# Kernel tuning notes

Hardware: AMD Instinct MI355X
Metric: run time of the kernel (lower is better)

Reference implementation:

```python
import jax, jax.numpy as jnp
import numpy as np

N_NODES = 75000
N_EDGES = 1200000
DIM = 64


def setup_inputs() -> dict:
    key = jax.random.key(0)
    ks = jax.random.split(key, 9)
    d_u = jax.random.normal(ks[0], (N_NODES, DIM), dtype=jnp.float32)
    p_u = jax.random.normal(ks[1], (N_NODES, DIM), dtype=jnp.float32)
    s = 1.0 / np.sqrt(DIM)
    w_q = jax.random.normal(ks[2], (DIM, DIM), dtype=jnp.float32) * s
    w_k = jax.random.normal(ks[3], (DIM, DIM), dtype=jnp.float32) * s
    w_v = jax.random.normal(ks[4], (DIM, DIM), dtype=jnp.float32) * s
    e1 = jax.random.normal(ks[5], (DIM,), dtype=jnp.float32) * s
    e2 = jax.random.normal(ks[6], (DIM,), dtype=jnp.float32) * s
    src = jax.random.randint(ks[7], (N_EDGES,), 0, N_NODES, dtype=jnp.int32)
    dst = jax.random.randint(ks[8], (N_EDGES,), 0, N_NODES, dtype=jnp.int32)
    return {"d_u": d_u, "p_u": p_u, "w_q": w_q, "w_k": w_k, "w_v": w_v,
            "e1": e1, "e2": e2, "src": src, "dst": dst}


def reference(d_u, p_u, w_q, w_k, w_v, e1, e2, src, dst):
    n_nodes = d_u.shape[0]
    # per-node edge scores: e1(w_k(p_u)) on src side, e2(w_q(d_u)) on dst side
    h_src = (p_u @ w_k.T) @ e1            # [N]
    h_dst = (d_u @ w_q.T) @ e2            # [N]
    # apply_edges(u_add_v): c_e = h_src[u] + h_dst[v], shape [E]
    c = h_src[src] + h_dst[dst]
    # EdgeWeightNorm(norm='right'): divide by sum of incoming edge weights at dst
    denom = jax.ops.segment_sum(c, dst, num_segments=n_nodes)  # [N]
    c = c / denom[dst]
    # update_all(u_mul_e, sum): messages w_v(p_u)[u] * c_e, summed at dst
    wv = p_u @ w_v.T                      # [N, D]
    msg = wv[src] * c[:, None]            # [E, D]
    out = jax.ops.segment_sum(msg, dst, num_segments=n_nodes)  # [N, D]
    return out
```

## Files before the change

### kernel.cpp

```cpp
#include <hip/hip_runtime.h>

#define N_NODES 75000
#define N_EDGES 1200000
#define DIM 64
#define SCAN_BLK 1024
#define N_SCAN_BLKS ((N_NODES + SCAN_BLK - 1) / SCAN_BLK)
#define NCOPY 8
#define HIST_BLKS ((N_EDGES + 1023) / 1024)
#define NW_BLKS 1024
#define FAT_BLKS (HIST_BLKS + NW_BLKS)

__device__ __forceinline__ float lane_bcf(float v, int l) {
    return __int_as_float(__builtin_amdgcn_readlane(__float_as_int(v), l));
}
__device__ __forceinline__ int lane_bci(int v, int l) {
    return __builtin_amdgcn_readlane(v, l);
}

__global__ __launch_bounds__(256, 4) void fat_kernel(
    const int* __restrict__ dst, int* __restrict__ cnt8, int* __restrict__ rank,
    const float* __restrict__ d_u, const float* __restrict__ p_u,
    const float* __restrict__ w_v, const float* __restrict__ w_q,
    const float* __restrict__ w_k,
    const float* __restrict__ e1, const float* __restrict__ e2,
    double* __restrict__ h_src, double* __restrict__ h_dst,
    float* __restrict__ wv_out) {

    if (blockIdx.x < HIST_BLKS) {
        int base = blockIdx.x << 10;
        int* mycnt = cnt8 + (size_t)(blockIdx.x & (NCOPY - 1)) * N_NODES;
        #pragma unroll
        for (int k = 0; k < 4; ++k) {
            int e = base + k * 256 + threadIdx.x;
            if (e < N_EDGES) {
                int d = __builtin_nontemporal_load(&dst[e]);
                int r = atomicAdd(&mycnt[d], 1);
                __builtin_nontemporal_store(r, &rank[e]);
            }
        }
        return;
    }

    __shared__ double al_sh[DIM];
    __shared__ double bl_sh[DIM];
    int lane = threadIdx.x & 63;

    if (threadIdx.x < DIM) {
        double al = 0.0, bl = 0.0;
        #pragma unroll 8
        for (int j = 0; j < DIM; ++j) {
            al += (double)e1[j] * (double)w_k[j * DIM + threadIdx.x];
            bl += (double)e2[j] * (double)w_q[j * DIM + threadIdx.x];
        }
        al_sh[threadIdx.x] = al;
        bl_sh[threadIdx.x] = bl;
    }

    float w[DIM];
    const float4* wr = (const float4*)(w_v + (size_t)lane * DIM);
    #pragma unroll
    for (int k = 0; k < DIM / 4; ++k) {
        float4 v = wr[k];
        w[4 * k + 0] = v.x; w[4 * k + 1] = v.y;
        w[4 * k + 2] = v.z; w[4 * k + 3] = v.w;
    }
    __syncthreads();
    double al = al_sh[lane];
    double bl = bl_sh[lane];

    int wave = ((blockIdx.x - HIST_BLKS) * 256 + threadIdx.x) >> 6;
    int nwaves = NW_BLKS * 4;

    for (int i = wave; i < N_NODES; i += nwaves) {
        float pl = __builtin_nontemporal_load(&p_u[(size_t)i * DIM + lane]);
        float dl = __builtin_nontemporal_load(&d_u[(size_t)i * DIM + lane]);

        double hs = (double)pl * al;
        #pragma unroll
        for (int off = 32; off > 0; off >>= 1) hs += __shfl_xor(hs, off, 64);
        double hd = (double)dl * bl;
        #pragma unroll
        for (int off = 32; off > 0; off >>= 1) hd += __shfl_xor(hd, off, 64);
        if (lane == 0) {
            __builtin_nontemporal_store(hs, &h_src[i]);
            __builtin_nontemporal_store(hd, &h_dst[i]);
        }

        float a0 = 0.f, a1 = 0.f, a2 = 0.f, a3 = 0.f;
        #pragma unroll
        for (int d = 0; d < DIM; d += 4) {
            a0 += w[d + 0] * lane_bcf(pl, d + 0);
            a1 += w[d + 1] * lane_bcf(pl, d + 1);
            a2 += w[d + 2] * lane_bcf(pl, d + 2);
            a3 += w[d + 3] * lane_bcf(pl, d + 3);
        }
        __builtin_nontemporal_store((a0 + a1) + (a2 + a3),
                                    &wv_out[(size_t)i * DIM + lane]);
    }
}

__global__ __launch_bounds__(SCAN_BLK) void scan1_kernel(
    int* __restrict__ cnt8, int* __restrict__ cnt,
    int* __restrict__ row, int* __restrict__ bsum) {
    __shared__ int sh[SCAN_BLK];
    int tid = threadIdx.x;
    int i = blockIdx.x * SCAN_BLK + tid;
    int v = 0;
    if (i < N_NODES) {
        int run = 0;
        #pragma unroll
        for (int c = 0; c < NCOPY; ++c) {
            int x = cnt8[(size_t)c * N_NODES + i];
            cnt8[(size_t)c * N_NODES + i] = run;
            run += x;
        }
        v = run;
        cnt[i] = run;
    }
    sh[tid] = v;
    __syncthreads();
    for (int off = 1; off < SCAN_BLK; off <<= 1) {
        int t = (tid >= off) ? sh[tid - off] : 0;
        __syncthreads();
        sh[tid] += t;
        __syncthreads();
    }
    if (i < N_NODES) row[i] = sh[tid] - v;
    if (tid == SCAN_BLK - 1) bsum[blockIdx.x] = sh[tid];
}

__global__ __launch_bounds__(256) void scan23_kernel(
    int* __restrict__ row, const int* __restrict__ bsum) {
    __shared__ int pref[N_SCAN_BLKS];
    int tid = threadIdx.x;
    if (tid == 0) {
        int run = 0;
        #pragma unroll 8
        for (int k = 0; k < N_SCAN_BLKS; ++k) { pref[k] = run; run += bsum[k]; }
    }
    __syncthreads();
    int i = blockIdx.x * 256 + tid;
    if (i >= N_NODES) return;
    row[i] += pref[i / SCAN_BLK];
}

__global__ __launch_bounds__(256) void build_kernel(
    const int* __restrict__ src, const int* __restrict__ dst,
    const int* __restrict__ row, const int* __restrict__ cnt8,
    const int* __restrict__ rank, int* __restrict__ csr_src) {
    int e = blockIdx.x * 256 + threadIdx.x;
    if (e >= N_EDGES) return;
    int d = dst[e];
    int copy = (e >> 10) & (NCOPY - 1);
    int pos = row[d] + cnt8[(size_t)copy * N_NODES + d] + rank[e];
    csr_src[pos] = src[e];
}

__global__ __launch_bounds__(256) void node_gather(
    const int* __restrict__ row, const int* __restrict__ cnt,
    const int* __restrict__ csr_src,
    const double* __restrict__ h_src, const double* __restrict__ h_dst,
    const float* __restrict__ wv, float* __restrict__ out) {
    int gtid = blockIdx.x * 256 + threadIdx.x;
    int node = gtid >> 6;
    int lane = threadIdx.x & 63;
    if (node >= N_NODES) return;

    int start = row[node];
    int deg = cnt[node];
    double hd = h_dst[node];

    if (deg <= 64) {
        int s0 = 0;
        double c0 = 0.0;
        if (lane < deg) {
            s0 = csr_src[start + lane];
            c0 = h_src[s0] + hd;
        }
        double r = c0;
        if (deg > 32) r += __shfl_xor(r, 32, 64);
        if (deg > 16) r += __shfl_xor(r, 16, 64);
        r += __shfl_xor(r, 8, 64);
        r += __shfl_xor(r, 4, 64);
        r += __shfl_xor(r, 2, 64);
        r += __shfl_xor(r, 1, 64);
        double inv = 1.0 / r;
        float cf0 = (lane < deg) ? (float)(c0 * inv) : 0.f;

        int g = lane >> 4;
        int sub = lane & 15;
        float ax = 0.f, ay = 0.f, az = 0.f, aw = 0.f;
        int rounds = (deg + 3) >> 2;
        int j = 0;
        for (; j + 2 <= rounds; j += 2) {
            int l0 = 4 * j + g;
            int l1 = l0 + 4;
            int   sA = __shfl(s0, l0, 64);
            float cA = __shfl(cf0, l0, 64);
            int   sB = __shfl(s0, l1, 64);
            float cB = __shfl(cf0, l1, 64);
            float4 vA = ((const float4*)(wv + (size_t)sA * DIM))[sub];
            float4 vB = ((const float4*)(wv + (size_t)sB * DIM))[sub];
            ax += vA.x * cA; ay += vA.y * cA; az += vA.z * cA; aw += vA.w * cA;
            ax += vB.x * cB; ay += vB.y * cB; az += vB.z * cB; aw += vB.w * cB;
        }
        if (j < rounds) {
            int l0 = 4 * j + g;
            int   sA = __shfl(s0, l0, 64);
            float cA = __shfl(cf0, l0, 64);
            float4 vA = ((const float4*)(wv + (size_t)sA * DIM))[sub];
            ax += vA.x * cA; ay += vA.y * cA; az += vA.z * cA; aw += vA.w * cA;
        }
        ax += __shfl_xor(ax, 16, 64); ay += __shfl_xor(ay, 16, 64);
        az += __shfl_xor(az, 16, 64); aw += __shfl_xor(aw, 16, 64);
        ax += __shfl_xor(ax, 32, 64); ay += __shfl_xor(ay, 32, 64);
        az += __shfl_xor(az, 32, 64); aw += __shfl_xor(aw, 32, 64);
        if (g == 0) {
            float4 o; o.x = ax; o.y = ay; o.z = az; o.w = aw;
            ((float4*)(out + (size_t)node * DIM))[sub] = o;
        }
    } else {
        double denom = 0.0;
        for (int base = 0; base < deg; base += 64) {
            int m = deg - base; if (m > 64) m = 64;
            double c = 0.0;
            if (lane < m) {
                int s = csr_src[start + base + lane];
                c = h_src[s] + hd;
            }
            #pragma unroll
            for (int off = 32; off > 0; off >>= 1) c += __shfl_xor(c, off, 64);
            denom += c;
        }
        double inv = 1.0 / denom;
        float acc = 0.f;
        for (int base = 0; base < deg; base += 64) {
            int m = deg - base; if (m > 64) m = 64;
            int s1 = 0; float cf1 = 0.f;
            if (lane < m) {
                s1 = csr_src[start + base + lane];
                cf1 = (float)((h_src[s1] + hd) * inv);
            }
            for (int j = 0; j < m; ++j) {
                int s = lane_bci(s1, j);
                float cf = lane_bcf(cf1, j);
                acc += wv[(size_t)s * DIM + lane] * cf;
            }
        }
        out[(size_t)node * DIM + lane] = acc;
    }
}

extern "C" void kernel_launch(void* const* d_in, const int* in_sizes, int n_in,
                              void* d_out, int out_size, void* d_ws, size_t ws_size,
                              hipStream_t stream) {
    const float* d_u = (const float*)d_in[0];
    const float* p_u = (const float*)d_in[1];
    const float* w_q = (const float*)d_in[2];
    const float* w_k = (const float*)d_in[3];
    const float* w_v = (const float*)d_in[4];
    const float* e1  = (const float*)d_in[5];
    const float* e2  = (const float*)d_in[6];
    const int*   src = (const int*)d_in[7];
    const int*   dst = (const int*)d_in[8];
    float* out = (float*)d_out;

    double* h_src  = (double*)d_ws;
    double* h_dst  = h_src + N_NODES;
    float*  wv     = (float*)(h_dst + N_NODES);
    int*    cnt    = (int*)(wv + (size_t)N_NODES * DIM);
    int*    row    = cnt + N_NODES;
    int*    bsum   = row + N_NODES;
    int*    cnt8   = bsum + 128;
    int*    rank   = cnt8 + (size_t)NCOPY * N_NODES;
    int*    csr_src= rank + N_EDGES;

    hipMemsetAsync(cnt8, 0, sizeof(int) * (size_t)NCOPY * N_NODES, stream);

    fat_kernel<<<FAT_BLKS, 256, 0, stream>>>(
        dst, cnt8, rank, d_u, p_u, w_v, w_q, w_k, e1, e2, h_src, h_dst, wv);

    scan1_kernel<<<N_SCAN_BLKS, SCAN_BLK, 0, stream>>>(cnt8, cnt, row, bsum);
    scan23_kernel<<<(N_NODES + 255) / 256, 256, 0, stream>>>(row, bsum);

    build_kernel<<<(N_EDGES + 255) / 256, 256, 0, stream>>>(
        src, dst, row, cnt8, rank, csr_src);

    node_gather<<<(N_NODES * 64 + 255) / 256, 256, 0, stream>>>(
        row, cnt, csr_src, h_src, h_dst, wv, out);
}
```

Before: 274.2 us.

## Use XCC-local histogram copies, interleave block roles, fuse scan passes

Histogram blocks now select their counter copy by the hardware XCC ID, so atomics from one chiplet stay on that chiplet's copy, and the copy index is packed into the rank's top bits for the build step. Histogram and node-work blocks are interleaved 2:1 so both kinds of work are spread across the device. The two scan kernels are merged into one single-pass scan where each block publishes its sum with a flag and later blocks spin on earlier ones. Nontemporal hints are removed in several places. The spin wait assumes earlier blocks are scheduled first, which risks a deadlock if they are not.

```diff
diff --git a/kernel.cpp b/kernel.cpp
--- a/kernel.cpp
+++ b/kernel.cpp
@@ -6,8 +6,8 @@
 #define SCAN_BLK 1024
 #define N_SCAN_BLKS ((N_NODES + SCAN_BLK - 1) / SCAN_BLK)
 #define NCOPY 8
-#define HIST_BLKS ((N_EDGES + 1023) / 1024)
-#define NW_BLKS 1024
+#define HIST_BLKS 1172
+#define NW_BLKS 586
 #define FAT_BLKS (HIST_BLKS + NW_BLKS)
 
 __device__ __forceinline__ float lane_bcf(float v, int l) {
@@ -26,16 +26,24 @@
     double* __restrict__ h_src, double* __restrict__ h_dst,
     float* __restrict__ wv_out) {
 
-    if (blockIdx.x < HIST_BLKS) {
-        int base = blockIdx.x << 10;
-        int* mycnt = cnt8 + (size_t)(blockIdx.x & (NCOPY - 1)) * N_NODES;
+    int b = blockIdx.x;
+    int g = b / 3;
+    int r = b - 3 * g;
+
+    if (r < 2) {
+        int hb = 2 * g + r;
+        int xcc;
+        asm volatile("s_getreg_b32 %0, hwreg(HW_REG_XCC_ID)" : "=s"(xcc));
+        xcc &= (NCOPY - 1);
+        int* mycnt = cnt8 + (size_t)xcc * N_NODES;
+        int tag = xcc << 28;
+        int base = hb << 10;
         #pragma unroll
         for (int k = 0; k < 4; ++k) {
             int e = base + k * 256 + threadIdx.x;
             if (e < N_EDGES) {
-                int d = __builtin_nontemporal_load(&dst[e]);
-                int r = atomicAdd(&mycnt[d], 1);
-                __builtin_nontemporal_store(r, &rank[e]);
+                int rr = atomicAdd(&mycnt[dst[e]], 1);
+                rank[e] = rr | tag;
             }
         }
         return;
@@ -68,12 +76,12 @@
     double al = al_sh[lane];
     double bl = bl_sh[lane];
 
-    int wave = ((blockIdx.x - HIST_BLKS) * 256 + threadIdx.x) >> 6;
+    int wave = (g * 256 + threadIdx.x) >> 6;
     int nwaves = NW_BLKS * 4;
 
     for (int i = wave; i < N_NODES; i += nwaves) {
-        float pl = __builtin_nontemporal_load(&p_u[(size_t)i * DIM + lane]);
-        float dl = __builtin_nontemporal_load(&d_u[(size_t)i * DIM + lane]);
+        float pl = p_u[(size_t)i * DIM + lane];
+        float dl = d_u[(size_t)i * DIM + lane];
 
         double hs = (double)pl * al;
         #pragma unroll
@@ -81,10 +89,7 @@
         double hd = (double)dl * bl;
         #pragma unroll
         for (int off = 32; off > 0; off >>= 1) hd += __shfl_xor(hd, off, 64);
-        if (lane == 0) {
-            __builtin_nontemporal_store(hs, &h_src[i]);
-            __builtin_nontemporal_store(hd, &h_dst[i]);
-        }
+        if (lane == 0) { h_src[i] = hs; h_dst[i] = hd; }
 
         float a0 = 0.f, a1 = 0.f, a2 = 0.f, a3 = 0.f;
         #pragma unroll
@@ -94,15 +99,15 @@
             a2 += w[d + 2] * lane_bcf(pl, d + 2);
             a3 += w[d + 3] * lane_bcf(pl, d + 3);
         }
-        __builtin_nontemporal_store((a0 + a1) + (a2 + a3),
-                                    &wv_out[(size_t)i * DIM + lane]);
-    }
-}
-
-__global__ __launch_bounds__(SCAN_BLK) void scan1_kernel(
+        wv_out[(size_t)i * DIM + lane] = (a0 + a1) + (a2 + a3);
+    }
+}
+
+__global__ __launch_bounds__(SCAN_BLK) void scan_kernel(
     int* __restrict__ cnt8, int* __restrict__ cnt,
-    int* __restrict__ row, int* __restrict__ bsum) {
+    int* __restrict__ row, unsigned int* __restrict__ pub) {
     __shared__ int sh[SCAN_BLK];
+    __shared__ int bpref;
     int tid = threadIdx.x;
     int i = blockIdx.x * SCAN_BLK + tid;
     int v = 0;
@@ -125,23 +130,22 @@
         sh[tid] += t;
         __syncthreads();
     }
-    if (i < N_NODES) row[i] = sh[tid] - v;
-    if (tid == SCAN_BLK - 1) bsum[blockIdx.x] = sh[tid];
-}
-
-__global__ __launch_bounds__(256) void scan23_kernel(
-    int* __restrict__ row, const int* __restrict__ bsum) {
-    __shared__ int pref[N_SCAN_BLKS];
-    int tid = threadIdx.x;
-    if (tid == 0) {
-        int run = 0;
-        #pragma unroll 8
-        for (int k = 0; k < N_SCAN_BLKS; ++k) { pref[k] = run; run += bsum[k]; }
+    int incl = sh[tid];
+    if (tid == SCAN_BLK - 1)
+        atomicExch(&pub[blockIdx.x], (unsigned)incl | 0x80000000u);
+    if (tid < 64) {
+        int s = 0;
+        for (int l = tid; l < (int)blockIdx.x; l += 64) {
+            unsigned x;
+            do { x = atomicAdd(&pub[l], 0u); } while (!(x & 0x80000000u));
+            s += (int)(x & 0x7FFFFFFFu);
+        }
+        #pragma unroll
+        for (int off = 32; off > 0; off >>= 1) s += __shfl_xor(s, off, 64);
+        if (tid == 0) bpref = s;
     }
     __syncthreads();
-    int i = blockIdx.x * 256 + tid;
-    if (i >= N_NODES) return;
-    row[i] += pref[i / SCAN_BLK];
+    if (i < N_NODES) row[i] = bpref + incl - v;
 }
 
 __global__ __launch_bounds__(256) void build_kernel(
@@ -151,9 +155,11 @@
     int e = blockIdx.x * 256 + threadIdx.x;
     if (e >= N_EDGES) return;
     int d = dst[e];
-    int copy = (e >> 10) & (NCOPY - 1);
-    int pos = row[d] + cnt8[(size_t)copy * N_NODES + d] + rank[e];
-    csr_src[pos] = src[e];
+    int rp = rank[e];
+    int copy = (rp >> 28) & (NCOPY - 1);
+    int r = rp & 0x0FFFFFFF;
+    int pos = row[d] + cnt8[(size_t)copy * N_NODES + d] + r;
+    __builtin_nontemporal_store(src[e], &csr_src[pos]);
 }
 
 __global__ __launch_bounds__(256) void node_gather(
@@ -270,18 +276,18 @@
     float*  wv     = (float*)(h_dst + N_NODES);
     int*    cnt    = (int*)(wv + (size_t)N_NODES * DIM);
     int*    row    = cnt + N_NODES;
-    int*    bsum   = row + N_NODES;
-    int*    cnt8   = bsum + 128;
-    int*    rank   = cnt8 + (size_t)NCOPY * N_NODES;
+    int*    cnt8   = row + N_NODES;
+    unsigned int* pub = (unsigned int*)(cnt8 + (size_t)NCOPY * N_NODES);
+    int*    rank   = (int*)pub + 128;
     int*    csr_src= rank + N_EDGES;
 
-    hipMemsetAsync(cnt8, 0, sizeof(int) * (size_t)NCOPY * N_NODES, stream);
+    hipMemsetAsync(cnt8, 0, sizeof(int) * ((size_t)NCOPY * N_NODES + 128),
+                   stream);
 
     fat_kernel<<<FAT_BLKS, 256, 0, stream>>>(
         dst, cnt8, rank, d_u, p_u, w_v, w_q, w_k, e1, e2, h_src, h_dst, wv);
 
-    scan1_kernel<<<N_SCAN_BLKS, SCAN_BLK, 0, stream>>>(cnt8, cnt, row, bsum);
-    scan23_kernel<<<(N_NODES + 255) / 256, 256, 0, stream>>>(row, bsum);
+    scan_kernel<<<N_SCAN_BLKS, SCAN_BLK, 0, stream>>>(cnt8, cnt, row, pub);
 
     build_kernel<<<(N_EDGES + 255) / 256, 256, 0, stream>>>(
         src, dst, row, cnt8, rank, csr_src);
```

Measured after the change: 272.2 us. No clear change (-0.7%).
